# Optimization experiments

Hardware: AMD Instinct MI355X
Metric: run time of the kernel (lower is better)

Reference implementation:

```python
import jax, jax.numpy as jnp
import numpy as np

NUM_AA, EMB_DIM = 20, 16
H1, H2 = 128, 128
K, EXCLUDE = 64, 3
R_ON, R_CUT = 10.0, 12.0
RBF_CENTERS = (5.0, 6.0, 7.0, 8.0, 9.0, 10.0, 11.0)
RBF_WIDTH = 0.5
M = len(RBF_CENTERS)


def setup_inputs() -> dict:
    key = jax.random.key(0)
    ks = jax.random.split(key, 10)
    B, L = 8, 2048
    R = jax.random.normal(ks[0], (B, L, 3), dtype=jnp.float32) * 10.0  # spread distances over RBF range
    seq = jax.random.randint(ks[1], (B, L), 0, NUM_AA)
    emb_table = jax.random.normal(ks[2], (NUM_AA, EMB_DIM), dtype=jnp.float32) * 0.1
    in_dim = 3 * EMB_DIM
    W1 = jax.random.normal(ks[3], (in_dim, H1), dtype=jnp.float32) / np.sqrt(in_dim)
    b1 = jnp.zeros((H1,), jnp.float32)
    W2 = jax.random.normal(ks[4], (H1, H2), dtype=jnp.float32) / np.sqrt(H1)
    b2 = jnp.zeros((H2,), jnp.float32)
    W3 = jax.random.normal(ks[5], (H2, M), dtype=jnp.float32) / np.sqrt(H2)
    b3 = jnp.zeros((M,), jnp.float32)
    centers = jnp.asarray(RBF_CENTERS, jnp.float32)
    widths = jnp.full((M,), RBF_WIDTH, jnp.float32)
    return {"R": R, "seq": seq, "emb_table": emb_table,
            "W1": W1, "b1": b1, "W2": W2, "b2": b2, "W3": W3, "b3": b3,
            "centers": centers, "widths": widths}


def topk_nonbonded_pairs(R, K, exclude):
    # R: (B, L, 3) -> r: (B, L, K) distances, j: (B, L, K) neighbor indices
    B, L, _ = R.shape
    diff = R[:, :, None, :] - R[:, None, :, :]            # (B, L, L, 3)
    D = jnp.sqrt(jnp.sum(diff * diff, axis=-1) + 1e-12)   # (B, L, L)
    idx = jnp.arange(L)
    bonded = jnp.abs(idx[:, None] - idx[None, :]) <= exclude  # excludes self too
    D = jnp.where(bonded[None], jnp.inf, D)
    neg, j = jax.lax.top_k(-D, K)                          # K smallest distances
    return -neg, j


def smooth_switch(r, r_on, r_cut):
    t = jnp.clip((r - r_on) / (r_cut - r_on), 0.0, 1.0)
    return 1.0 - t * t * (3.0 - 2.0 * t)  # smoothstep down: 1 below r_on, 0 above r_cut


def distance_features(r, centers, widths):
    d = r[..., None] - centers  # (B, L, K, M)
    return jnp.exp(-(d * d) / (2.0 * widths * widths))


def reference(R, seq, emb_table, W1, b1, W2, b2, W3, b3, centers, widths):
    e = emb_table[seq]                                     # (B, L, d)
    r, j = topk_nonbonded_pairs(R, K, EXCLUDE)             # (B, L, K)
    e_j = jnp.take_along_axis(e[:, :, None, :], j[..., None], axis=1)  # wrong axis semantics avoided below
    # gather neighbor embeddings: e_j[b, i, k] = e[b, j[b, i, k]]
    e_j = jnp.take_along_axis(e[:, None, :, :].repeat(1, axis=1), j[..., None], axis=2) if False else \
          jnp.take_along_axis(e[:, :, None, :].transpose(0, 2, 1, 3).repeat(1, axis=0), j[..., None], axis=2) if False else \
          jax.vmap(lambda eb, jb: eb[jb])(e, j)            # (B, L, K, d)
    e_i = jnp.broadcast_to(e[:, :, None, :], e_j.shape)
    pair_feat = jnp.concatenate([e_i, e_j, e_i * e_j], axis=-1)  # (B, L, K, 3d)
    h = jax.nn.relu(pair_feat @ W1 + b1)
    h = jax.nn.relu(h @ W2 + b2)
    w = jax.nn.softplus(h @ W3 + b3)                       # (B, L, K, M)
    phi = distance_features(r, centers, widths)            # (B, L, K, M)
    att = -jnp.sum(w * phi, axis=-1)                       # (B, L, K)
    sw = smooth_switch(r, R_ON, R_CUT)
    return jnp.sum(att * sw, axis=(1, 2))                  # (B,)
```

## Files before the change

### kernel.cpp

```cpp
#include <hip/hip_runtime.h>
#include <math.h>

#define LSEQ 2048
#define KNB 64
#define BATCH 8
#define MRBF 7
#define NPAIRS (BATCH*LSEQ*KNB)
#define NTILES (NPAIRS/128)
#define XST 68
#define HST 136
#define NBINS 2048
#define D2CUT 144.0f
#define KSCALE (2047.0f/144.0f)

typedef __attribute__((ext_vector_type(8))) short short8;
typedef __attribute__((ext_vector_type(4))) float floatx4;

__device__ __forceinline__ unsigned short f2bf(float f) {
    unsigned u = __float_as_uint(f);
    u += 0x7fffu + ((u >> 16) & 1u);
    return (unsigned short)(u >> 16);
}
__device__ __forceinline__ unsigned pkbf(float a, float b) {
    return ((__float_as_uint(a) + 0x8000u) >> 16) |
           ((__float_as_uint(b) + 0x8000u) & 0xffff0000u);
}

__global__ __launch_bounds__(256) void topk_kernel(
    const float* __restrict__ R, int* __restrict__ nbr)
{
    const int bi = blockIdx.x;
    const int i  = bi & (LSEQ - 1);
    const int bL = bi & ~(LSEQ - 1);
    const int tid  = threadIdx.x;
    const int lane = tid & 63;
    const int wv   = tid >> 6;

    __shared__ unsigned hist[NBINS];
    __shared__ unsigned cumw[4];
    __shared__ int s_B;
    __shared__ unsigned s_below;
    __shared__ int outPos, candCnt, fillCnt;
    __shared__ float cand_d2[512];
    __shared__ int   cand_idx[512];

    #pragma unroll
    for (int u = 0; u < 8; u++) hist[tid + 256*u] = 0u;
    if (tid == 0) { outPos = 0; candCnt = 0; fillCnt = 0; }

    const float xi = R[bi*3+0], yi = R[bi*3+1], zi = R[bi*3+2];
    float d2r[8]; int keyr[8];
    __syncthreads();

    #pragma unroll
    for (int u = 0; u < 8; u++) {
        int j = tid + 256*u;
        float dx = xi - R[(bL+j)*3+0];
        float dy = yi - R[(bL+j)*3+1];
        float dz = zi - R[(bL+j)*3+2];
        float d2 = dx*dx + dy*dy + dz*dz;
        int dd = j - i; dd = dd < 0 ? -dd : dd;
        if (dd <= 3) d2 = __uint_as_float(0x7f800000u);
        int key = (d2 < D2CUT) ? (int)(d2 * KSCALE) : (NBINS - 1);
        d2r[u] = d2; keyr[u] = key;
        atomicAdd(&hist[key], 1u);
    }
    __syncthreads();

    unsigned s = 0;
    #pragma unroll
    for (int v = 0; v < 8; v++) s += hist[8*tid + v];
    unsigned inc = s;
    #pragma unroll
    for (int off = 1; off < 64; off <<= 1) {
        unsigned n = __shfl_up(inc, off, 64);
        if (lane >= off) inc += n;
    }
    if (lane == 63) cumw[wv] = inc;
    __syncthreads();
    unsigned woff = 0;
    for (int w = 0; w < wv; w++) woff += cumw[w];
    unsigned excl = woff + inc - s;
    if (excl < 64u && 64u <= excl + s) {
        unsigned c = excl;
        #pragma unroll
        for (int v = 0; v < 8; v++) {
            unsigned h = hist[8*tid + v];
            if (c < 64u && 64u <= c + h) { s_B = 8*tid + v; s_below = c; }
            c += h;
        }
    }
    __syncthreads();
    const int B = s_B;
    const int need = 64 - (int)s_below;
    const int outBase = bi * KNB;

    #pragma unroll
    for (int u = 0; u < 8; u++) {
        int j = tid + 256*u;
        int k = keyr[u];
        if (k < B) {
            int pos = atomicAdd(&outPos, 1);
            nbr[outBase + pos] = j;
        } else if (k == B) {
            if (B == NBINS - 1) {
                if (d2r[u] < 3.0e38f) {
                    int t = atomicAdd(&fillCnt, 1);
                    if (t < need) { int pos = atomicAdd(&outPos, 1); nbr[outBase + pos] = j; }
                }
            } else {
                int c = atomicAdd(&candCnt, 1);
                if (c < 512) { cand_d2[c] = d2r[u]; cand_idx[c] = j; }
            }
        }
    }
    __syncthreads();
    if (B != NBINS - 1) {
        int c = candCnt; if (c > 512) c = 512;
        for (int ci = tid; ci < c; ci += 256) {
            float dv = cand_d2[ci]; int jv = cand_idx[ci];
            int rank = 0;
            for (int x = 0; x < c; x++) {
                float dx2 = cand_d2[x]; int jx = cand_idx[x];
                rank += (dx2 < dv) || (dx2 == dv && jx < jv);
            }
            if (rank < need) { int pos = atomicAdd(&outPos, 1); nbr[outBase + pos] = jv; }
        }
    }
}

__global__ __launch_bounds__(256, 3) void mlp_mfma_kernel(
    const float* __restrict__ R, const int* __restrict__ seq,
    const float* __restrict__ emb,
    const float* __restrict__ W1, const float* __restrict__ b1,
    const float* __restrict__ W2, const float* __restrict__ b2,
    const float* __restrict__ W3, const float* __restrict__ b3,
    const float* __restrict__ centers, const float* __restrict__ widths,
    const int* __restrict__ nbr, float* __restrict__ out)
{
    __shared__ __align__(16) unsigned short Xs[128*XST];
    __shared__ __align__(16) unsigned short Hs[128*HST];
    __shared__ float r_s[128];
    __shared__ float bacc[BATCH];

    const int tid  = threadIdx.x;
    const int lane = tid & 63;
    const int wv   = tid >> 6;
    const int l15  = lane & 15;
    const int q    = lane >> 4;

    short8 w1f[2][2], w2f[2][4], w3f[4];
    float b1v[2][4], b2v[2][4];
    #pragma unroll
    for (int mtl = 0; mtl < 2; mtl++) {
        int m = (2*wv + mtl)*16 + l15;
        #pragma unroll
        for (int d = 0; d < 4; d++) {
            b1v[mtl][d] = b1[(2*wv + mtl)*16 + q*4 + d];
            b2v[mtl][d] = b2[(2*wv + mtl)*16 + q*4 + d];
        }
        #pragma unroll
        for (int kt = 0; kt < 2; kt++)
            #pragma unroll
            for (int j = 0; j < 8; j++) {
                int k = kt*32 + q*8 + j;
                w1f[mtl][kt][j] = (short)((k < 48) ? f2bf(W1[k*128 + m]) : 0);
            }
        #pragma unroll
        for (int kt = 0; kt < 4; kt++)
            #pragma unroll
            for (int j = 0; j < 8; j++) {
                int k = kt*32 + q*8 + j;
                w2f[mtl][kt][j] = (short)f2bf(W2[k*128 + m]);
            }
    }
    #pragma unroll
    for (int kt = 0; kt < 4; kt++)
        #pragma unroll
        for (int j = 0; j < 8; j++) {
            int k = kt*32 + q*8 + j;
            w3f[kt][j] = (short)((l15 < MRBF) ? f2bf(W3[k*MRBF + l15]) : 0);
        }
    float b3v[4], cen[4], i2w[4];
    #pragma unroll
    for (int d = 0; d < 4; d++) {
        int rb = q*4 + d;
        bool ok = rb < MRBF;
        b3v[d] = ok ? b3[rb] : 0.f;
        cen[d] = ok ? centers[rb] : 0.f;
        float wd = ok ? widths[rb] : 1.f;
        i2w[d] = 0.5f / (wd*wd);
    }
    if (tid < BATCH) bacc[tid] = 0.f;

    for (int tile = blockIdx.x; tile < NTILES; tile += gridDim.x) {
        __syncthreads();

        {
            int pl = tid >> 1, half = tid & 1;
            int p  = tile*128 + pl;
            int bi = p >> 6;
            int b  = p >> 17;
            int jn = nbr[p];
            int rowj = (b << 11) + jn;
            int si = seq[bi], sj = seq[rowj];
            const float* ei = emb + si*16 + half*8;
            const float* ej = emb + sj*16 + half*8;
            float a0[8], c0[8];
            #pragma unroll
            for (int f = 0; f < 8; f++) { a0[f] = ei[f]; c0[f] = ej[f]; }
            int base = pl*XST + half*8;
            uint2* pe = (uint2*)&Xs[base];
            pe[0] = make_uint2(pkbf(a0[0],a0[1]), pkbf(a0[2],a0[3]));
            pe[1] = make_uint2(pkbf(a0[4],a0[5]), pkbf(a0[6],a0[7]));
            uint2* pn = (uint2*)&Xs[base + 16];
            pn[0] = make_uint2(pkbf(c0[0],c0[1]), pkbf(c0[2],c0[3]));
            pn[1] = make_uint2(pkbf(c0[4],c0[5]), pkbf(c0[6],c0[7]));
            uint2* pp = (uint2*)&Xs[base + 32];
            pp[0] = make_uint2(pkbf(a0[0]*c0[0],a0[1]*c0[1]), pkbf(a0[2]*c0[2],a0[3]*c0[3]));
            pp[1] = make_uint2(pkbf(a0[4]*c0[4],a0[5]*c0[5]), pkbf(a0[6]*c0[6],a0[7]*c0[7]));
            uint2* pz = (uint2*)&Xs[base + 48];
            pz[0] = make_uint2(0u, 0u);
            pz[1] = make_uint2(0u, 0u);
            if (!half) {
                float dx = R[bi*3+0] - R[rowj*3+0];
                float dy = R[bi*3+1] - R[rowj*3+1];
                float dz = R[bi*3+2] - R[rowj*3+2];
                r_s[pl] = sqrtf(dx*dx + dy*dy + dz*dz + 1e-12f);
            }
        }
        __syncthreads();

        #pragma unroll
        for (int nt = 0; nt < 8; nt++) {
            const unsigned long long* px =
                (const unsigned long long*)&Xs[(nt*16 + l15)*XST];
            short8 xf[2];
            #pragma unroll
            for (int kt = 0; kt < 2; kt++) {
                union { short8 s; unsigned long long u[2]; } t;
                t.u[0] = px[kt*8 + 0];
                t.u[1] = px[kt*8 + 1];
                xf[kt] = t.s;
            }
            #pragma unroll
            for (int mtl = 0; mtl < 2; mtl++) {
                floatx4 acc = {0.f, 0.f, 0.f, 0.f};
                acc = __builtin_amdgcn_mfma_f32_16x16x32_bf16(w1f[mtl][0], xf[0], acc, 0, 0, 0);
                acc = __builtin_amdgcn_mfma_f32_16x16x32_bf16(w1f[mtl][1], xf[1], acc, 0, 0, 0);
                float v0 = fmaxf(acc[0] + b1v[mtl][0], 0.f);
                float v1 = fmaxf(acc[1] + b1v[mtl][1], 0.f);
                float v2 = fmaxf(acc[2] + b1v[mtl][2], 0.f);
                float v3 = fmaxf(acc[3] + b1v[mtl][3], 0.f);
                *(uint2*)&Hs[(nt*16 + l15)*HST + (2*wv + mtl)*16 + q*4] =
                    make_uint2(pkbf(v0,v1), pkbf(v2,v3));
            }
        }
        __syncthreads();

        uint2 h2p[8][2];
        #pragma unroll
        for (int nt = 0; nt < 8; nt++) {
            const unsigned short* ph = &Hs[(nt*16 + l15)*HST];
            short8 hf[4];
            #pragma unroll
            for (int kt = 0; kt < 4; kt++)
                hf[kt] = *(const short8*)&ph[kt*32];
            #pragma unroll
            for (int mtl = 0; mtl < 2; mtl++) {
                floatx4 acc = {0.f, 0.f, 0.f, 0.f};
                acc = __builtin_amdgcn_mfma_f32_16x16x32_bf16(w2f[mtl][0], hf[0], acc, 0, 0, 0);
                acc = __builtin_amdgcn_mfma_f32_16x16x32_bf16(w2f[mtl][1], hf[1], acc, 0, 0, 0);
                acc = __builtin_amdgcn_mfma_f32_16x16x32_bf16(w2f[mtl][2], hf[2], acc, 0, 0, 0);
                acc = __builtin_amdgcn_mfma_f32_16x16x32_bf16(w2f[mtl][3], hf[3], acc, 0, 0, 0);
                float v0 = fmaxf(acc[0] + b2v[mtl][0], 0.f);
                float v1 = fmaxf(acc[1] + b2v[mtl][1], 0.f);
                float v2 = fmaxf(acc[2] + b2v[mtl][2], 0.f);
                float v3 = fmaxf(acc[3] + b2v[mtl][3], 0.f);
                h2p[nt][mtl] = make_uint2(pkbf(v0,v1), pkbf(v2,v3));
            }
        }
        __syncthreads();
        #pragma unroll
        for (int nt = 0; nt < 8; nt++)
            #pragma unroll
            for (int mtl = 0; mtl < 2; mtl++)
                *(uint2*)&Hs[(nt*16 + l15)*HST + (2*wv + mtl)*16 + q*4] = h2p[nt][mtl];
        __syncthreads();

        float esum = 0.f;
        #pragma unroll
        for (int ntl = 0; ntl < 2; ntl++) {
            int nt = 2*wv + ntl;
            const unsigned short* ph = &Hs[(nt*16 + l15)*HST];
            floatx4 acc = {0.f, 0.f, 0.f, 0.f};
            #pragma unroll
            for (int kt = 0; kt < 4; kt++) {
                short8 hf = *(const short8*)&ph[kt*32];
                acc = __builtin_amdgcn_mfma_f32_16x16x32_bf16(w3f[kt], hf, acc, 0, 0, 0);
            }
            float rr = r_s[nt*16 + l15];
            if (rr < 12.0f) {
                float att = 0.f;
                #pragma unroll
                for (int d = 0; d < 4; d++) {
                    if (q*4 + d < MRBF) {
                        float x = acc[d] + b3v[d];
                        float sp = fmaxf(x, 0.f) + __logf(1.f + __expf(-fabsf(x)));
                        float dd = rr - cen[d];
                        att += sp * __expf(-dd*dd*i2w[d]);
                    }
                }
                att += __shfl_xor(att, 16, 64);
                att += __shfl_xor(att, 32, 64);
                float t = fminf(fmaxf((rr - 10.f)*0.5f, 0.f), 1.f);
                float sw = 1.f - t*t*(3.f - 2.f*t);
                esum -= att * sw;
            }
        }
        #pragma unroll
        for (int off = 1; off < 64; off <<= 1)
            esum += __shfl_xor(esum, off, 64);
        if (lane == 0) atomicAdd(&bacc[tile >> 10], esum * 0.25f);
    }
    __syncthreads();
    if (tid < BATCH) atomicAdd(&out[tid], bacc[tid]);
}

extern "C" void kernel_launch(void* const* d_in, const int* in_sizes, int n_in,
                              void* d_out, int out_size, void* d_ws, size_t ws_size,
                              hipStream_t stream) {
    const float* R       = (const float*)d_in[0];
    const int*   seq     = (const int*)  d_in[1];
    const float* emb     = (const float*)d_in[2];
    const float* W1      = (const float*)d_in[3];
    const float* b1      = (const float*)d_in[4];
    const float* W2      = (const float*)d_in[5];
    const float* b2      = (const float*)d_in[6];
    const float* W3      = (const float*)d_in[7];
    const float* b3      = (const float*)d_in[8];
    const float* centers = (const float*)d_in[9];
    const float* widths  = (const float*)d_in[10];
    float* out = (float*)d_out;
    int*   nbr = (int*)d_ws;

    hipMemsetAsync(d_out, 0, out_size * sizeof(float), stream);

    topk_kernel<<<BATCH*LSEQ, 256, 0, stream>>>(R, nbr);
    mlp_mfma_kernel<<<2048, 256, 0, stream>>>(R, seq, emb, W1, b1, W2, b2, W3, b3,
                                              centers, widths, nbr, out);
}
```

Baseline: 299.6 us.

## Rewrite top-k to batch four rows per block and MLP to register-only waves

The top-k kernel now loads a batch's coordinates into LDS and handles four query rows per block. It uses 256-bin histograms per row and recomputes distances instead of keeping them in registers. The MLP kernel drops the LDS staging and block barriers: each wave holds all 128 output columns of the weights in registers, processes 32 pairs per group, and passes activations between layers with lane shuffles. It also prefetches the next group's gathers. The costs are high register pressure (launch bounds 1 wave per SIMD), a coarser histogram that may produce more tie-bin candidates, and many shuffles per layer.

```diff
diff --git a/kernel.cpp b/kernel.cpp
--- a/kernel.cpp
+++ b/kernel.cpp
@@ -5,16 +5,13 @@
 #define KNB 64
 #define BATCH 8
 #define MRBF 7
-#define NPAIRS (BATCH*LSEQ*KNB)
-#define NTILES (NPAIRS/128)
-#define XST 68
-#define HST 136
-#define NBINS 2048
-#define D2CUT 144.0f
-#define KSCALE (2047.0f/144.0f)
+#define TOTPAIR (BATCH*LSEQ*KNB)
+#define NGROUP (TOTPAIR/32)
+#define BSCALE (255.0f/144.0f)
 
 typedef __attribute__((ext_vector_type(8))) short short8;
 typedef __attribute__((ext_vector_type(4))) float floatx4;
+typedef __attribute__((ext_vector_type(4))) int int4v;
 
 __device__ __forceinline__ unsigned short f2bf(float f) {
     unsigned u = __float_as_uint(f);
@@ -22,114 +19,177 @@
     return (unsigned short)(u >> 16);
 }
 __device__ __forceinline__ unsigned pkbf(float a, float b) {
-    return ((__float_as_uint(a) + 0x8000u) >> 16) |
-           ((__float_as_uint(b) + 0x8000u) & 0xffff0000u);
+    return __builtin_amdgcn_perm(__float_as_uint(b) + 0x8000u,
+                                 __float_as_uint(a) + 0x8000u, 0x07060302u);
 }
 
 __global__ __launch_bounds__(256) void topk_kernel(
     const float* __restrict__ R, int* __restrict__ nbr)
 {
-    const int bi = blockIdx.x;
-    const int i  = bi & (LSEQ - 1);
-    const int bL = bi & ~(LSEQ - 1);
-    const int tid  = threadIdx.x;
+    __shared__ __align__(16) float Rl[LSEQ*3];
+    __shared__ unsigned hist[4*256];
+    __shared__ float cand_d2[4][128];
+    __shared__ int   cand_j[4][128];
+    __shared__ int s_B[4], s_need[4];
+    __shared__ int outPos[4], candCnt[4], fillCnt[4];
+
+    const int tid = threadIdx.x;
     const int lane = tid & 63;
-    const int wv   = tid >> 6;
-
-    __shared__ unsigned hist[NBINS];
-    __shared__ unsigned cumw[4];
-    __shared__ int s_B;
-    __shared__ unsigned s_below;
-    __shared__ int outPos, candCnt, fillCnt;
-    __shared__ float cand_d2[512];
-    __shared__ int   cand_idx[512];
-
-    #pragma unroll
-    for (int u = 0; u < 8; u++) hist[tid + 256*u] = 0u;
-    if (tid == 0) { outPos = 0; candCnt = 0; fillCnt = 0; }
-
-    const float xi = R[bi*3+0], yi = R[bi*3+1], zi = R[bi*3+2];
-    float d2r[8]; int keyr[8];
+    const int wv = tid >> 6;
+    const int b  = blockIdx.x >> 9;
+    const int i0 = (blockIdx.x & 511) << 2;
+    const float* Rb = R + b*LSEQ*3;
+
+    for (int u = tid; u < LSEQ*3/4; u += 256)
+        *(float4*)&Rl[u*4] = *(const float4*)&Rb[u*4];
+    #pragma unroll
+    for (int u = 0; u < 4; u++) hist[tid + 256*u] = 0u;
+    if (tid < 4) { outPos[tid] = 0; candCnt[tid] = 0; fillCnt[tid] = 0; }
     __syncthreads();
 
+    float xi[4], yi[4], zi[4];
+    #pragma unroll
+    for (int c = 0; c < 4; c++) {
+        xi[c] = Rl[(i0+c)*3+0]; yi[c] = Rl[(i0+c)*3+1]; zi[c] = Rl[(i0+c)*3+2];
+    }
+
     #pragma unroll
     for (int u = 0; u < 8; u++) {
-        int j = tid + 256*u;
-        float dx = xi - R[(bL+j)*3+0];
-        float dy = yi - R[(bL+j)*3+1];
-        float dz = zi - R[(bL+j)*3+2];
-        float d2 = dx*dx + dy*dy + dz*dz;
-        int dd = j - i; dd = dd < 0 ? -dd : dd;
-        if (dd <= 3) d2 = __uint_as_float(0x7f800000u);
-        int key = (d2 < D2CUT) ? (int)(d2 * KSCALE) : (NBINS - 1);
-        d2r[u] = d2; keyr[u] = key;
-        atomicAdd(&hist[key], 1u);
+        int j = tid + (u << 8);
+        float px = Rl[3*j], py = Rl[3*j+1], pz = Rl[3*j+2];
+        #pragma unroll
+        for (int c = 0; c < 4; c++) {
+            float dx = xi[c]-px, dy = yi[c]-py, dz = zi[c]-pz;
+            float d2 = dx*dx + dy*dy + dz*dz;
+            int dd = j - (i0+c); dd = dd < 0 ? -dd : dd;
+            if (dd > 3 && d2 < 144.0f)
+                atomicAdd(&hist[c*256 + (int)(d2*BSCALE)], 1u);
+        }
     }
     __syncthreads();
 
-    unsigned s = 0;
-    #pragma unroll
-    for (int v = 0; v < 8; v++) s += hist[8*tid + v];
-    unsigned inc = s;
-    #pragma unroll
-    for (int off = 1; off < 64; off <<= 1) {
-        unsigned n = __shfl_up(inc, off, 64);
-        if (lane >= off) inc += n;
-    }
-    if (lane == 63) cumw[wv] = inc;
+    {
+        unsigned h4[4]; unsigned s = 0;
+        #pragma unroll
+        for (int v = 0; v < 4; v++) { h4[v] = hist[wv*256 + lane*4 + v]; s += h4[v]; }
+        unsigned inc = s;
+        #pragma unroll
+        for (int off = 1; off < 64; off <<= 1) {
+            unsigned n = __shfl_up(inc, off, 64);
+            if (lane >= off) inc += n;
+        }
+        unsigned tot = __shfl(inc, 63, 64);
+        unsigned excl = inc - s;
+        if (tot < 64u) {
+            if (lane == 0) { s_B[wv] = 255; s_need[wv] = 64 - (int)tot; }
+        } else if (excl < 64u && 64u <= inc) {
+            unsigned cc = excl;
+            #pragma unroll
+            for (int v = 0; v < 4; v++) {
+                if (cc < 64u && 64u <= cc + h4[v]) { s_B[wv] = lane*4+v; s_need[wv] = 64 - (int)cc; }
+                cc += h4[v];
+            }
+        }
+    }
     __syncthreads();
-    unsigned woff = 0;
-    for (int w = 0; w < wv; w++) woff += cumw[w];
-    unsigned excl = woff + inc - s;
-    if (excl < 64u && 64u <= excl + s) {
-        unsigned c = excl;
-        #pragma unroll
-        for (int v = 0; v < 8; v++) {
-            unsigned h = hist[8*tid + v];
-            if (c < 64u && 64u <= c + h) { s_B = 8*tid + v; s_below = c; }
-            c += h;
+
+    #pragma unroll
+    for (int u = 0; u < 8; u++) {
+        int j = tid + (u << 8);
+        float px = Rl[3*j], py = Rl[3*j+1], pz = Rl[3*j+2];
+        #pragma unroll
+        for (int c = 0; c < 4; c++) {
+            float dx = xi[c]-px, dy = yi[c]-py, dz = zi[c]-pz;
+            float d2 = dx*dx + dy*dy + dz*dz;
+            int dd = j - (i0+c); dd = dd < 0 ? -dd : dd;
+            if (dd <= 3) continue;
+            int B = s_B[c];
+            int obase = (b*LSEQ + i0 + c)*KNB;
+            if (d2 < 144.0f) {
+                int key = (int)(d2*BSCALE);
+                if (key < B) {
+                    int pos = atomicAdd(&outPos[c], 1);
+                    nbr[obase + pos] = j;
+                } else if (key == B) {
+                    int cc = atomicAdd(&candCnt[c], 1);
+                    if (cc < 128) { cand_d2[c][cc] = d2; cand_j[c][cc] = j; }
+                }
+            } else if (B == 255) {
+                int t = atomicAdd(&fillCnt[c], 1);
+                if (t < s_need[c]) {
+                    int pos = atomicAdd(&outPos[c], 1);
+                    nbr[obase + pos] = j;
+                }
+            }
         }
     }
     __syncthreads();
-    const int B = s_B;
-    const int need = 64 - (int)s_below;
-    const int outBase = bi * KNB;
-
-    #pragma unroll
-    for (int u = 0; u < 8; u++) {
-        int j = tid + 256*u;
-        int k = keyr[u];
-        if (k < B) {
-            int pos = atomicAdd(&outPos, 1);
-            nbr[outBase + pos] = j;
-        } else if (k == B) {
-            if (B == NBINS - 1) {
-                if (d2r[u] < 3.0e38f) {
-                    int t = atomicAdd(&fillCnt, 1);
-                    if (t < need) { int pos = atomicAdd(&outPos, 1); nbr[outBase + pos] = j; }
-                }
-            } else {
-                int c = atomicAdd(&candCnt, 1);
-                if (c < 512) { cand_d2[c] = d2r[u]; cand_idx[c] = j; }
-            }
-        }
-    }
-    __syncthreads();
-    if (B != NBINS - 1) {
-        int c = candCnt; if (c > 512) c = 512;
-        for (int ci = tid; ci < c; ci += 256) {
-            float dv = cand_d2[ci]; int jv = cand_idx[ci];
-            int rank = 0;
-            for (int x = 0; x < c; x++) {
-                float dx2 = cand_d2[x]; int jx = cand_idx[x];
-                rank += (dx2 < dv) || (dx2 == dv && jx < jv);
-            }
-            if (rank < need) { int pos = atomicAdd(&outPos, 1); nbr[outBase + pos] = jv; }
-        }
-    }
-}
-
-__global__ __launch_bounds__(256, 3) void mlp_mfma_kernel(
+
+    {
+        int B = s_B[wv];
+        if (B != 255) {
+            int c = candCnt[wv]; if (c > 128) c = 128;
+            int need = s_need[wv];
+            int obase = (b*LSEQ + i0 + wv)*KNB;
+            for (int ci = lane; ci < c; ci += 64) {
+                float dv = cand_d2[wv][ci]; int jv = cand_j[wv][ci];
+                int rank = 0;
+                for (int x = 0; x < c; x++) {
+                    float dx2 = cand_d2[wv][x]; int jx = cand_j[wv][x];
+                    rank += (dx2 < dv) || (dx2 == dv && jx < jv);
+                }
+                if (rank < need) {
+                    int pos = atomicAdd(&outPos[wv], 1);
+                    nbr[obase + pos] = jv;
+                }
+            }
+        }
+    }
+}
+
+__device__ __forceinline__ short8 gather_frag(unsigned pA0, unsigned pA1,
+                                              unsigned pB0, unsigned pB1,
+                                              int src0, bool hi)
+{
+    int a0 = __shfl((int)pA0, src0,      64);
+    int a1 = __shfl((int)pA1, src0,      64);
+    int a2 = __shfl((int)pA0, src0 + 16, 64);
+    int a3 = __shfl((int)pA1, src0 + 16, 64);
+    int c0 = __shfl((int)pB0, src0,      64);
+    int c1 = __shfl((int)pB1, src0,      64);
+    int c2 = __shfl((int)pB0, src0 + 16, 64);
+    int c3 = __shfl((int)pB1, src0 + 16, 64);
+    int4v r;
+    r[0] = hi ? c0 : a0; r[1] = hi ? c1 : a1;
+    r[2] = hi ? c2 : a2; r[3] = hi ? c3 : a3;
+    return __builtin_bit_cast(short8, r);
+}
+
+__device__ __forceinline__ void ldgrp(int g, int q, int l15,
+    const int* __restrict__ nbr, const int* __restrict__ seq,
+    const float* __restrict__ emb, const float* __restrict__ R,
+    float v[2][8], float rc[2][6])
+{
+    #pragma unroll
+    for (int t = 0; t < 2; t++) {
+        int p = g*32 + t*16 + l15;
+        int bi = p >> 6;
+        int bb = p >> 17;
+        int j  = nbr[p];
+        int rowj = (bb << 11) + j;
+        int srow = (q < 2) ? bi : rowj;
+        int s = seq[srow];
+        const float* ep = emb + s*16 + (q & 1)*8;
+        float4 e0 = *(const float4*)ep;
+        float4 e1 = *(const float4*)(ep + 4);
+        v[t][0]=e0.x; v[t][1]=e0.y; v[t][2]=e0.z; v[t][3]=e0.w;
+        v[t][4]=e1.x; v[t][5]=e1.y; v[t][6]=e1.z; v[t][7]=e1.w;
+        rc[t][0]=R[bi*3+0];   rc[t][1]=R[bi*3+1];   rc[t][2]=R[bi*3+2];
+        rc[t][3]=R[rowj*3+0]; rc[t][4]=R[rowj*3+1]; rc[t][5]=R[rowj*3+2];
+    }
+}
+
+__global__ __launch_bounds__(256, 1) void mlp_kernel(
     const float* __restrict__ R, const int* __restrict__ seq,
     const float* __restrict__ emb,
     const float* __restrict__ W1, const float* __restrict__ b1,
@@ -138,193 +198,172 @@
     const float* __restrict__ centers, const float* __restrict__ widths,
     const int* __restrict__ nbr, float* __restrict__ out)
 {
-    __shared__ __align__(16) unsigned short Xs[128*XST];
-    __shared__ __align__(16) unsigned short Hs[128*HST];
-    __shared__ float r_s[128];
-    __shared__ float bacc[BATCH];
-
-    const int tid  = threadIdx.x;
+    const int tid = threadIdx.x;
     const int lane = tid & 63;
-    const int wv   = tid >> 6;
-    const int l15  = lane & 15;
-    const int q    = lane >> 4;
-
-    short8 w1f[2][2], w2f[2][4], w3f[4];
-    float b1v[2][4], b2v[2][4];
-    #pragma unroll
-    for (int mtl = 0; mtl < 2; mtl++) {
-        int m = (2*wv + mtl)*16 + l15;
+    const int wv = tid >> 6;
+    const int l15 = lane & 15;
+    const int q = lane >> 4;
+
+    short8 w1f[8][2], w2f[8][4], w3f[4];
+    float b1v[8][4], b2v[8][4];
+    #pragma unroll
+    for (int mtl = 0; mtl < 8; mtl++) {
+        int m = mtl*16 + l15;
         #pragma unroll
         for (int d = 0; d < 4; d++) {
-            b1v[mtl][d] = b1[(2*wv + mtl)*16 + q*4 + d];
-            b2v[mtl][d] = b2[(2*wv + mtl)*16 + q*4 + d];
+            b1v[mtl][d] = b1[mtl*16 + q*4 + d];
+            b2v[mtl][d] = b2[mtl*16 + q*4 + d];
         }
         #pragma unroll
         for (int kt = 0; kt < 2; kt++)
             #pragma unroll
-            for (int j = 0; j < 8; j++) {
-                int k = kt*32 + q*8 + j;
-                w1f[mtl][kt][j] = (short)((k < 48) ? f2bf(W1[k*128 + m]) : 0);
+            for (int jj = 0; jj < 8; jj++) {
+                int k = kt*32 + q*8 + jj;
+                w1f[mtl][kt][jj] = (short)((k < 48) ? f2bf(W1[k*128 + m]) : 0);
             }
         #pragma unroll
         for (int kt = 0; kt < 4; kt++)
             #pragma unroll
-            for (int j = 0; j < 8; j++) {
-                int k = kt*32 + q*8 + j;
-                w2f[mtl][kt][j] = (short)f2bf(W2[k*128 + m]);
+            for (int jj = 0; jj < 8; jj++) {
+                int k = kt*32 + q*8 + jj;
+                w2f[mtl][kt][jj] = (short)f2bf(W2[k*128 + m]);
             }
     }
     #pragma unroll
     for (int kt = 0; kt < 4; kt++)
         #pragma unroll
-        for (int j = 0; j < 8; j++) {
-            int k = kt*32 + q*8 + j;
-            w3f[kt][j] = (short)((l15 < MRBF) ? f2bf(W3[k*MRBF + l15]) : 0);
-        }
-    float b3v[4], cen[4], i2w[4];
+        for (int jj = 0; jj < 8; jj++) {
+            int k = kt*32 + q*8 + jj;
+            w3f[kt][jj] = (short)((l15 < MRBF) ? f2bf(W3[k*MRBF + l15]) : 0);
+        }
+    float b3C[4], cen[4], i2w[4];
     #pragma unroll
     for (int d = 0; d < 4; d++) {
         int rb = q*4 + d;
         bool ok = rb < MRBF;
-        b3v[d] = ok ? b3[rb] : 0.f;
+        b3C[d] = ok ? b3[rb] : 0.f;
         cen[d] = ok ? centers[rb] : 0.f;
         float wd = ok ? widths[rb] : 1.f;
         i2w[d] = 0.5f / (wd*wd);
     }
-    if (tid < BATCH) bacc[tid] = 0.f;
-
-    for (int tile = blockIdx.x; tile < NTILES; tile += gridDim.x) {
-        __syncthreads();
-
-        {
-            int pl = tid >> 1, half = tid & 1;
-            int p  = tile*128 + pl;
-            int bi = p >> 6;
-            int b  = p >> 17;
-            int jn = nbr[p];
-            int rowj = (b << 11) + jn;
-            int si = seq[bi], sj = seq[rowj];
-            const float* ei = emb + si*16 + half*8;
-            const float* ej = emb + sj*16 + half*8;
-            float a0[8], c0[8];
-            #pragma unroll
-            for (int f = 0; f < 8; f++) { a0[f] = ei[f]; c0[f] = ej[f]; }
-            int base = pl*XST + half*8;
-            uint2* pe = (uint2*)&Xs[base];
-            pe[0] = make_uint2(pkbf(a0[0],a0[1]), pkbf(a0[2],a0[3]));
-            pe[1] = make_uint2(pkbf(a0[4],a0[5]), pkbf(a0[6],a0[7]));
-            uint2* pn = (uint2*)&Xs[base + 16];
-            pn[0] = make_uint2(pkbf(c0[0],c0[1]), pkbf(c0[2],c0[3]));
-            pn[1] = make_uint2(pkbf(c0[4],c0[5]), pkbf(c0[6],c0[7]));
-            uint2* pp = (uint2*)&Xs[base + 32];
-            pp[0] = make_uint2(pkbf(a0[0]*c0[0],a0[1]*c0[1]), pkbf(a0[2]*c0[2],a0[3]*c0[3]));
-            pp[1] = make_uint2(pkbf(a0[4]*c0[4],a0[5]*c0[5]), pkbf(a0[6]*c0[6],a0[7]*c0[7]));
-            uint2* pz = (uint2*)&Xs[base + 48];
-            pz[0] = make_uint2(0u, 0u);
-            pz[1] = make_uint2(0u, 0u);
-            if (!half) {
-                float dx = R[bi*3+0] - R[rowj*3+0];
-                float dy = R[bi*3+1] - R[rowj*3+1];
-                float dz = R[bi*3+2] - R[rowj*3+2];
-                r_s[pl] = sqrtf(dx*dx + dy*dy + dz*dz + 1e-12f);
-            }
-        }
-        __syncthreads();
-
-        #pragma unroll
-        for (int nt = 0; nt < 8; nt++) {
-            const unsigned long long* px =
-                (const unsigned long long*)&Xs[(nt*16 + l15)*XST];
-            short8 xf[2];
-            #pragma unroll
-            for (int kt = 0; kt < 2; kt++) {
-                union { short8 s; unsigned long long u[2]; } t;
-                t.u[0] = px[kt*8 + 0];
-                t.u[1] = px[kt*8 + 1];
-                xf[kt] = t.s;
-            }
-            #pragma unroll
-            for (int mtl = 0; mtl < 2; mtl++) {
-                floatx4 acc = {0.f, 0.f, 0.f, 0.f};
-                acc = __builtin_amdgcn_mfma_f32_16x16x32_bf16(w1f[mtl][0], xf[0], acc, 0, 0, 0);
-                acc = __builtin_amdgcn_mfma_f32_16x16x32_bf16(w1f[mtl][1], xf[1], acc, 0, 0, 0);
-                float v0 = fmaxf(acc[0] + b1v[mtl][0], 0.f);
-                float v1 = fmaxf(acc[1] + b1v[mtl][1], 0.f);
-                float v2 = fmaxf(acc[2] + b1v[mtl][2], 0.f);
-                float v3 = fmaxf(acc[3] + b1v[mtl][3], 0.f);
-                *(uint2*)&Hs[(nt*16 + l15)*HST + (2*wv + mtl)*16 + q*4] =
-                    make_uint2(pkbf(v0,v1), pkbf(v2,v3));
-            }
-        }
-        __syncthreads();
-
-        uint2 h2p[8][2];
-        #pragma unroll
-        for (int nt = 0; nt < 8; nt++) {
-            const unsigned short* ph = &Hs[(nt*16 + l15)*HST];
+
+    const int src0 = l15 + 32*(q & 1);
+    const bool hi = (q >> 1) != 0;
+    const int GS = gridDim.x * 4;
+    const int gw = blockIdx.x*4 + wv;
+
+    float vcur[2][8], rcur[2][6];
+    float esum = 0.f;
+    int bcur = -1;
+    if (gw < NGROUP) { ldgrp(gw, q, l15, nbr, seq, emb, R, vcur, rcur); bcur = gw >> 12; }
+
+    for (int g = gw; g < NGROUP; g += GS) {
+        int gn = g + GS;
+        float vnx[2][8], rnx[2][6];
+        bool hn = gn < NGROUP;
+        if (hn) ldgrp(gn, q, l15, nbr, seq, emb, R, vnx, rnx);
+
+        int bb = g >> 12;
+        if (bb != bcur) {
+            float s_ = esum;
+            #pragma unroll
+            for (int off = 1; off < 64; off <<= 1) s_ += __shfl_xor(s_, off, 64);
+            if (lane == 0) atomicAdd(&out[bcur], s_*0.25f);
+            esum = 0.f; bcur = bb;
+        }
+
+        #pragma unroll
+        for (int t = 0; t < 2; t++) {
+            int4v xi0;
+            xi0[0] = (int)pkbf(vcur[t][0], vcur[t][1]);
+            xi0[1] = (int)pkbf(vcur[t][2], vcur[t][3]);
+            xi0[2] = (int)pkbf(vcur[t][4], vcur[t][5]);
+            xi0[3] = (int)pkbf(vcur[t][6], vcur[t][7]);
+            short8 x0 = __builtin_bit_cast(short8, xi0);
+            float pr[8];
+            #pragma unroll
+            for (int f = 0; f < 8; f++)
+                pr[f] = vcur[t][f] * __shfl_xor(vcur[t][f], 32, 64);
+            bool lo2 = q < 2;
+            int4v xi1;
+            xi1[0] = lo2 ? (int)pkbf(pr[0], pr[1]) : 0;
+            xi1[1] = lo2 ? (int)pkbf(pr[2], pr[3]) : 0;
+            xi1[2] = lo2 ? (int)pkbf(pr[4], pr[5]) : 0;
+            xi1[3] = lo2 ? (int)pkbf(pr[6], pr[7]) : 0;
+            short8 x1 = __builtin_bit_cast(short8, xi1);
+
+            unsigned pk1[8][2];
+            #pragma unroll
+            for (int mtl = 0; mtl < 8; mtl++) {
+                floatx4 acc = {b1v[mtl][0], b1v[mtl][1], b1v[mtl][2], b1v[mtl][3]};
+                acc = __builtin_amdgcn_mfma_f32_16x16x32_bf16(w1f[mtl][0], x0, acc, 0, 0, 0);
+                acc = __builtin_amdgcn_mfma_f32_16x16x32_bf16(w1f[mtl][1], x1, acc, 0, 0, 0);
+                pk1[mtl][0] = pkbf(fmaxf(acc[0],0.f), fmaxf(acc[1],0.f));
+                pk1[mtl][1] = pkbf(fmaxf(acc[2],0.f), fmaxf(acc[3],0.f));
+            }
             short8 hf[4];
             #pragma unroll
             for (int kt = 0; kt < 4; kt++)
-                hf[kt] = *(const short8*)&ph[kt*32];
-            #pragma unroll
-            for (int mtl = 0; mtl < 2; mtl++) {
-                floatx4 acc = {0.f, 0.f, 0.f, 0.f};
+                hf[kt] = gather_frag(pk1[2*kt][0], pk1[2*kt][1],
+                                     pk1[2*kt+1][0], pk1[2*kt+1][1], src0, hi);
+            unsigned pk2[8][2];
+            #pragma unroll
+            for (int mtl = 0; mtl < 8; mtl++) {
+                floatx4 acc = {b2v[mtl][0], b2v[mtl][1], b2v[mtl][2], b2v[mtl][3]};
                 acc = __builtin_amdgcn_mfma_f32_16x16x32_bf16(w2f[mtl][0], hf[0], acc, 0, 0, 0);
                 acc = __builtin_amdgcn_mfma_f32_16x16x32_bf16(w2f[mtl][1], hf[1], acc, 0, 0, 0);
                 acc = __builtin_amdgcn_mfma_f32_16x16x32_bf16(w2f[mtl][2], hf[2], acc, 0, 0, 0);
                 acc = __builtin_amdgcn_mfma_f32_16x16x32_bf16(w2f[mtl][3], hf[3], acc, 0, 0, 0);
-                float v0 = fmaxf(acc[0] + b2v[mtl][0], 0.f);
-                float v1 = fmaxf(acc[1] + b2v[mtl][1], 0.f);
-                float v2 = fmaxf(acc[2] + b2v[mtl][2], 0.f);
-                float v3 = fmaxf(acc[3] + b2v[mtl][3], 0.f);
-                h2p[nt][mtl] = make_uint2(pkbf(v0,v1), pkbf(v2,v3));
-            }
-        }
-        __syncthreads();
-        #pragma unroll
-        for (int nt = 0; nt < 8; nt++)
-            #pragma unroll
-            for (int mtl = 0; mtl < 2; mtl++)
-                *(uint2*)&Hs[(nt*16 + l15)*HST + (2*wv + mtl)*16 + q*4] = h2p[nt][mtl];
-        __syncthreads();
-
-        float esum = 0.f;
-        #pragma unroll
-        for (int ntl = 0; ntl < 2; ntl++) {
-            int nt = 2*wv + ntl;
-            const unsigned short* ph = &Hs[(nt*16 + l15)*HST];
-            floatx4 acc = {0.f, 0.f, 0.f, 0.f};
-            #pragma unroll
-            for (int kt = 0; kt < 4; kt++) {
-                short8 hf = *(const short8*)&ph[kt*32];
-                acc = __builtin_amdgcn_mfma_f32_16x16x32_bf16(w3f[kt], hf, acc, 0, 0, 0);
-            }
-            float rr = r_s[nt*16 + l15];
-            if (rr < 12.0f) {
-                float att = 0.f;
+                pk2[mtl][0] = pkbf(fmaxf(acc[0],0.f), fmaxf(acc[1],0.f));
+                pk2[mtl][1] = pkbf(fmaxf(acc[2],0.f), fmaxf(acc[3],0.f));
+            }
+            short8 h2[4];
+            #pragma unroll
+            for (int kt = 0; kt < 4; kt++)
+                h2[kt] = gather_frag(pk2[2*kt][0], pk2[2*kt][1],
+                                     pk2[2*kt+1][0], pk2[2*kt+1][1], src0, hi);
+            floatx4 a3 = {b3C[0], b3C[1], b3C[2], b3C[3]};
+            #pragma unroll
+            for (int kt = 0; kt < 4; kt++)
+                a3 = __builtin_amdgcn_mfma_f32_16x16x32_bf16(w3f[kt], h2[kt], a3, 0, 0, 0);
+
+            float dx = rcur[t][0]-rcur[t][3];
+            float dy = rcur[t][1]-rcur[t][4];
+            float dz = rcur[t][2]-rcur[t][5];
+            float r = sqrtf(dx*dx + dy*dy + dz*dz + 1e-12f);
+            float att = 0.f;
+            #pragma unroll
+            for (int d = 0; d < 4; d++) {
+                if (q*4 + d < MRBF) {
+                    float x = a3[d];
+                    float sp = fmaxf(x, 0.f) + __logf(1.f + __expf(-fabsf(x)));
+                    float df = r - cen[d];
+                    att += sp * __expf(-df*df*i2w[d]);
+                }
+            }
+            att += __shfl_xor(att, 16, 64);
+            att += __shfl_xor(att, 32, 64);
+            float tt = fminf(fmaxf((r - 10.f)*0.5f, 0.f), 1.f);
+            float sw = 1.f - tt*tt*(3.f - 2.f*tt);
+            esum -= att * sw;
+        }
+
+        if (hn) {
+            #pragma unroll
+            for (int t = 0; t < 2; t++) {
                 #pragma unroll
-                for (int d = 0; d < 4; d++) {
-                    if (q*4 + d < MRBF) {
-                        float x = acc[d] + b3v[d];
-                        float sp = fmaxf(x, 0.f) + __logf(1.f + __expf(-fabsf(x)));
-                        float dd = rr - cen[d];
-                        att += sp * __expf(-dd*dd*i2w[d]);
-                    }
-                }
-                att += __shfl_xor(att, 16, 64);
-                att += __shfl_xor(att, 32, 64);
-                float t = fminf(fmaxf((rr - 10.f)*0.5f, 0.f), 1.f);
-                float sw = 1.f - t*t*(3.f - 2.f*t);
-                esum -= att * sw;
-            }
-        }
-        #pragma unroll
-        for (int off = 1; off < 64; off <<= 1)
-            esum += __shfl_xor(esum, off, 64);
-        if (lane == 0) atomicAdd(&bacc[tile >> 10], esum * 0.25f);
-    }
-    __syncthreads();
-    if (tid < BATCH) atomicAdd(&out[tid], bacc[tid]);
+                for (int f = 0; f < 8; f++) vcur[t][f] = vnx[t][f];
+                #pragma unroll
+                for (int f = 0; f < 6; f++) rcur[t][f] = rnx[t][f];
+            }
+        }
+    }
+    if (bcur >= 0) {
+        float s_ = esum;
+        #pragma unroll
+        for (int off = 1; off < 64; off <<= 1) s_ += __shfl_xor(s_, off, 64);
+        if (lane == 0) atomicAdd(&out[bcur], s_*0.25f);
+    }
 }
 
 extern "C" void kernel_launch(void* const* d_in, const int* in_sizes, int n_in,
@@ -346,7 +385,7 @@
 
     hipMemsetAsync(d_out, 0, out_size * sizeof(float), stream);
 
-    topk_kernel<<<BATCH*LSEQ, 256, 0, stream>>>(R, nbr);
-    mlp_mfma_kernel<<<2048, 256, 0, stream>>>(R, seq, emb, W1, b1, W2, b2, W3, b3,
-                                              centers, widths, nbr, out);
-}
+    topk_kernel<<<BATCH*(LSEQ/4), 256, 0, stream>>>(R, nbr);
+    mlp_kernel<<<512, 256, 0, stream>>>(R, seq, emb, W1, b1, W2, b2, W3, b3,
+                                        centers, widths, nbr, out);
+}
```

New measurement: 432.5 us. +44.4%, slower.
